# Performance work log

Measured on AMD Instinct MI355X. Metric: run time of the kernel, lower is better.

Reference implementation:

```python
import jax, jax.numpy as jnp
import numpy as np

B, S, D, H = 2, 2048, 1024, 16
HD = D // H  # head_size = 64

def setup_inputs() -> dict:
    key = jax.random.key(0)
    ks = jax.random.split(key, 8)
    sc = 0.02
    return {
        "q": jax.random.normal(ks[0], (B, S, D), jnp.float32),
        "k": jax.random.normal(ks[1], (B, S, D), jnp.float32),
        "v": jax.random.normal(ks[2], (B, S, D), jnp.float32),
        "padding_mask": jnp.zeros((B, 1, 1, S), jnp.float32),
        "Wq": jax.random.normal(ks[3], (D, D), jnp.float32) * sc,
        "bq": jnp.zeros((D,), jnp.float32),
        "Wk": jax.random.normal(ks[4], (D, D), jnp.float32) * sc,
        "bk": jnp.zeros((D,), jnp.float32),
        "Wv": jax.random.normal(ks[5], (D, D), jnp.float32) * sc,
        "bv": jnp.zeros((D,), jnp.float32),
        "Wo": jax.random.normal(ks[6], (D, D), jnp.float32) * sc,
        "bo": jnp.zeros((D,), jnp.float32),
    }

def reference(q, k, v, padding_mask, Wq, bq, Wk, bk, Wv, bv, Wo, bo):
    b = q.shape[0]
    qh = (q @ Wq + bq).reshape(b, -1, H, HD)
    kh = (k @ Wk + bk).reshape(b, -1, H, HD)
    vh = (v @ Wv + bv).reshape(b, -1, H, HD)
    # [B, H, Sq, Sk] scores, materialized as in the original
    qk = jnp.einsum('bjhd,bkhd->bhjk', qh, kh) / jnp.sqrt(jnp.float32(HD))
    qk = qk + padding_mask * -1e12
    attn = jax.nn.softmax(qk, axis=-1)
    qkv = jnp.einsum('bhjk,bkhd->bjhd', attn, vh).reshape(b, -1, D)
    return qkv @ Wo + bo
```

## Files before the change

### kernel.cpp

```cpp
#include <hip/hip_runtime.h>
#include <math.h>

typedef __bf16 bf16_t;
typedef __bf16 bf16x8 __attribute__((ext_vector_type(8)));
typedef __bf16 bf16x4v __attribute__((ext_vector_type(4)));
typedef float f32x4 __attribute__((ext_vector_type(4)));

#define LOG2E 1.4426950408889634f

#if __has_builtin(__builtin_amdgcn_exp2f)
#define EXP2F(x) __builtin_amdgcn_exp2f(x)
#else
#define EXP2F(x) exp2f(x)
#endif

typedef __attribute__((address_space(1))) const unsigned int g_u32;
typedef __attribute__((address_space(3))) unsigned int l_u32;
__device__ __forceinline__ void load_lds_16B(const void* g, void* l){
  __builtin_amdgcn_global_load_lds((g_u32*)g, (l_u32*)l, 16, 0, 0);
}

__global__ __launch_bounds__(256) void wtrans4_kernel(const float* __restrict__ Wq,
                                                      const float* __restrict__ Wk,
                                                      const float* __restrict__ Wv,
                                                      const float* __restrict__ Wo,
                                                      bf16_t* __restrict__ Wcat,
                                                      bf16_t* __restrict__ Wot){
  __shared__ float T[32][33];
  int z = blockIdx.z;
  const float* W = (z == 0) ? Wq : (z == 1) ? Wk : (z == 2) ? Wv : Wo;
  bf16_t* dst = (z < 3) ? (Wcat + (size_t)z * 1024 * 1024) : Wot;
  int x = threadIdx.x, y = threadIdx.y;
  int k0 = blockIdx.y * 32, n0 = blockIdx.x * 32;
  #pragma unroll
  for (int i = 0; i < 4; i++) T[y + 8*i][x] = W[(size_t)(k0 + y + 8*i) * 1024 + n0 + x];
  __syncthreads();
  #pragma unroll
  for (int i = 0; i < 4; i++) dst[(size_t)(n0 + y + 8*i) * 1024 + k0 + x] = (bf16_t)T[x][y + 8*i];
}

__global__ __launch_bounds__(256) void gemm_qkv(const float* __restrict__ qi,
                                                const float* __restrict__ ki,
                                                const float* __restrict__ vi,
                                                const bf16_t* __restrict__ Wcat,
                                                const float* __restrict__ bq,
                                                const float* __restrict__ bk,
                                                const float* __restrict__ bv,
                                                bf16_t* __restrict__ Cqkv){
  const int K = 1024, CS = 3072;
  __shared__ __align__(16) float  Asf[128*32];
  __shared__ __align__(16) bf16_t Bs[128*32];
  int tid = threadIdx.x, wave = tid >> 6, lane = tid & 63;
  int l16 = lane & 15, lq = lane >> 4;
  int n0g = blockIdx.x * 128;
  int seg = n0g >> 10;
  const float* A    = (seg == 0) ? qi : (seg == 1) ? ki : vi;
  const float* bias = (seg == 0) ? bq : (seg == 1) ? bk : bv;
  float scale = (seg == 0) ? 0.125f : 1.0f;
  int m0 = blockIdx.y * 128;
  int wm = (wave >> 1) * 64, wn = (wave & 1) * 64;
  int cposR = lq ^ ((l16 >> 2) & 3);
  int ca0 = (2*lq)     ^ (l16 & 7);
  int ca1 = (2*lq + 1) ^ (l16 & 7);
  f32x4 acc[4][4] = {};
  for (int kt = 0; kt < K; kt += 32){
    __syncthreads();
    #pragma unroll
    for (int i = 0; i < 4; i++){
      int u = tid + 256*i;
      int r = u >> 3, cpos = u & 7, cg = cpos ^ (r & 7);
      load_lds_16B(&A[(size_t)(m0 + r) * K + kt + cg*4], (char*)Asf + (wave*64 + 256*i)*16);
    }
    #pragma unroll
    for (int i = 0; i < 2; i++){
      int u = tid + 256*i;
      int r = u >> 2, cpos = u & 3, cg = cpos ^ ((r >> 2) & 3);
      load_lds_16B(&Wcat[(size_t)(n0g + r) * K + kt + cg*8], (char*)Bs + (wave*64 + 256*i)*16);
    }
    __syncthreads();
    bf16x8 af[4], bfr[4];
    #pragma unroll
    for (int t = 0; t < 4; t++){
      int row = wm + t*16 + l16;
      f32x4 x0 = *reinterpret_cast<f32x4*>(&Asf[row*32 + ca0*4]);
      f32x4 x1 = *reinterpret_cast<f32x4*>(&Asf[row*32 + ca1*4]);
      bf16x8 a;
      a[0] = (bf16_t)x0[0]; a[1] = (bf16_t)x0[1]; a[2] = (bf16_t)x0[2]; a[3] = (bf16_t)x0[3];
      a[4] = (bf16_t)x1[0]; a[5] = (bf16_t)x1[1]; a[6] = (bf16_t)x1[2]; a[7] = (bf16_t)x1[3];
      af[t] = a;
    }
    #pragma unroll
    for (int t = 0; t < 4; t++) bfr[t] = *reinterpret_cast<bf16x8*>(&Bs[(wn + t*16 + l16)*32 + cposR*8]);
    #pragma unroll
    for (int ti = 0; ti < 4; ti++)
      #pragma unroll
      for (int tj = 0; tj < 4; tj++)
        acc[ti][tj] = __builtin_amdgcn_mfma_f32_16x16x32_bf16(af[ti], bfr[tj], acc[ti][tj], 0, 0, 0);
  }
  #pragma unroll
  for (int ti = 0; ti < 4; ti++){
    #pragma unroll
    for (int tj = 0; tj < 4; tj++){
      int col = n0g + wn + tj*16 + l16;
      float bvv = bias[col & 1023];
      #pragma unroll
      for (int r = 0; r < 4; r++){
        int row = m0 + wm + ti*16 + lq*4 + r;
        Cqkv[(size_t)row * CS + col] = (bf16_t)((acc[ti][tj][r] + bvv) * scale);
      }
    }
  }
}

__global__ __launch_bounds__(256) void gemm_out(const bf16_t* __restrict__ A,
                                                const bf16_t* __restrict__ Bt,
                                                const float* __restrict__ bias,
                                                float* __restrict__ C){
  const int K = 1024, N = 1024;
  __shared__ __align__(16) bf16_t As[128*32];
  __shared__ __align__(16) bf16_t Bs[64*32];
  int tid = threadIdx.x, wave = tid >> 6, lane = tid & 63;
  int l16 = lane & 15, lq = lane >> 4;
  int m0 = blockIdx.y * 128, n0 = blockIdx.x * 64;
  int wm = wave * 32;
  int cposR = lq ^ ((l16 >> 2) & 3);
  f32x4 acc[2][4] = {};
  for (int kt = 0; kt < K; kt += 32){
    __syncthreads();
    #pragma unroll
    for (int i = 0; i < 2; i++){
      int u = tid + 256*i;
      int r = u >> 2, cpos = u & 3, cg = cpos ^ ((r >> 2) & 3);
      load_lds_16B(&A[(size_t)(m0 + r) * K + kt + cg*8], (char*)As + (wave*64 + 256*i)*16);
    }
    {
      int r = tid >> 2, cpos = tid & 3, cg = cpos ^ ((r >> 2) & 3);
      load_lds_16B(&Bt[(size_t)(n0 + r) * K + kt + cg*8], (char*)Bs + (wave*64)*16);
    }
    __syncthreads();
    bf16x8 af[2], bfr[4];
    #pragma unroll
    for (int t = 0; t < 2; t++) af[t]  = *reinterpret_cast<bf16x8*>(&As[(wm + t*16 + l16)*32 + cposR*8]);
    #pragma unroll
    for (int t = 0; t < 4; t++) bfr[t] = *reinterpret_cast<bf16x8*>(&Bs[(t*16 + l16)*32 + cposR*8]);
    #pragma unroll
    for (int ti = 0; ti < 2; ti++)
      #pragma unroll
      for (int tj = 0; tj < 4; tj++)
        acc[ti][tj] = __builtin_amdgcn_mfma_f32_16x16x32_bf16(af[ti], bfr[tj], acc[ti][tj], 0, 0, 0);
  }
  #pragma unroll
  for (int ti = 0; ti < 2; ti++){
    #pragma unroll
    for (int tj = 0; tj < 4; tj++){
      int col = n0 + tj*16 + l16;
      float bvv = bias[col];
      #pragma unroll
      for (int r = 0; r < 4; r++){
        int row = m0 + wm + ti*16 + lq*4 + r;
        C[(size_t)row * N + col] = acc[ti][tj][r] + bvv;
      }
    }
  }
}

__global__ __launch_bounds__(256) void vtrans_kernel(const bf16_t* __restrict__ qkv,
                                                     bf16_t* __restrict__ Vt){
  __shared__ bf16_t T[64][72];
  int tid = threadIdx.x;
  int s0 = blockIdx.x * 64, h = blockIdx.y, b = blockIdx.z;
  #pragma unroll
  for (int i = 0; i < 2; i++){
    int u = tid + 256*i;
    int r = u >> 3, c = (u & 7) * 8;
    *reinterpret_cast<uint4*>(&T[r][c]) =
      *reinterpret_cast<const uint4*>(&qkv[(size_t)(b*2048 + s0 + r) * 3072 + 2048 + h*64 + c]);
  }
  __syncthreads();
  #pragma unroll
  for (int i = 0; i < 2; i++){
    int u = tid + 256*i;
    int d = u >> 3, cs = (u & 7) * 8;
    bf16_t t8[8];
    #pragma unroll
    for (int j = 0; j < 8; j++) t8[j] = T[cs + j][d];
    *reinterpret_cast<uint4*>(&Vt[(size_t)((b*16 + h)*64 + d) * 2048 + s0 + cs]) =
      *reinterpret_cast<uint4*>(t8);
  }
}

__global__ __launch_bounds__(256) void attn_kernel(const bf16_t* __restrict__ qkv,
                                                   const bf16_t* __restrict__ vt,
                                                   const float* __restrict__ mask,
                                                   bf16_t* __restrict__ ctx){
  const int S = 2048, DS = 3072, D = 1024, HD = 64;
  __shared__ __align__(16) char smem[67584];
  bf16_t* Qs  = (bf16_t*)smem;
  bf16_t* Ps  = (bf16_t*)smem;
  bf16_t* Ks  = (bf16_t*)(smem + 34816);
  bf16_t* Vts = (bf16_t*)(smem + 51200);
  int tid = threadIdx.x, wave = tid >> 6, lane = tid & 63;
  int l16 = lane & 15, lq = lane >> 4;
  int qt = blockIdx.x, h = blockIdx.y, b = blockIdx.z;
  const bf16_t* Qg = qkv + (size_t)b*S*DS + h*HD;
  const bf16_t* Kg = qkv + (size_t)b*S*DS + 1024 + h*HD;
  const bf16_t* Vg = vt + (size_t)(b*16 + h)*HD*S;

  #pragma unroll
  for (int i = 0; i < 4; i++){
    int u = tid + 256*i;
    int r = u >> 3, cpos = u & 7, cg = cpos ^ (r & 7);
    load_lds_16B(&Qg[(size_t)(qt*128 + r) * DS + cg*8], smem + (wave*64 + 256*i)*16);
  }
  __syncthreads();
  bf16x8 qf[2][2];
  #pragma unroll
  for (int ti = 0; ti < 2; ti++)
    #pragma unroll
    for (int kk = 0; kk < 2; kk++){
      int row = wave*32 + ti*16 + l16;
      int cpos = (kk*4 + lq) ^ (l16 & 7);
      qf[ti][kk] = *reinterpret_cast<bf16x8*>(&Qs[row*64 + cpos*8]);
    }
  f32x4 o[2][4] = {};
  f32x4 ol[2] = {};
  bf16x8 ones;
  #pragma unroll
  for (int j = 0; j < 8; j++) ones[j] = (bf16_t)1.0f;

  for (int kt = 0; kt < S; kt += 128){
    __syncthreads();
    #pragma unroll
    for (int i = 0; i < 4; i++){
      int u = tid + 256*i;
      int r = u >> 3, cpos = u & 7, cg = cpos ^ (r & 7);
      load_lds_16B(&Kg[(size_t)(kt + r) * DS + cg*8], (char*)Ks + (wave*64 + 256*i)*16);
    }
    #pragma unroll
    for (int i = 0; i < 4; i++){
      int u = tid + 256*i;
      int r = u >> 4, cpos = u & 15, cg = cpos ^ (r & 15);
      load_lds_16B(&Vg[(size_t)r * S + kt + cg*8], (char*)Vts + (wave*64 + 256*i)*16);
    }
    __syncthreads();

    f32x4 sc[2][8];
    #pragma unroll
    for (int kk = 0; kk < 2; kk++){
      bf16x8 kf[8];
      #pragma unroll
      for (int tj = 0; tj < 8; tj++){
        int row = tj*16 + l16;
        int cpos = (kk*4 + lq) ^ (l16 & 7);
        kf[tj] = *reinterpret_cast<bf16x8*>(&Ks[row*64 + cpos*8]);
      }
      #pragma unroll
      for (int ti = 0; ti < 2; ti++)
        #pragma unroll
        for (int tj = 0; tj < 8; tj++){
          if (kk == 0){
            f32x4 z = {0.f, 0.f, 0.f, 0.f};
            sc[ti][tj] = __builtin_amdgcn_mfma_f32_16x16x32_bf16(kf[tj], qf[ti][0], z, 0, 0, 0);
          } else {
            sc[ti][tj] = __builtin_amdgcn_mfma_f32_16x16x32_bf16(kf[tj], qf[ti][1], sc[ti][tj], 0, 0, 0);
          }
        }
    }
    float4 mb4[8];
    #pragma unroll
    for (int tj = 0; tj < 8; tj++){
      float4 mv = *reinterpret_cast<const float4*>(&mask[(size_t)b*S + kt + tj*16 + lq*4]);
      mb4[tj].x = mv.x * (-1e12f * LOG2E); mb4[tj].y = mv.y * (-1e12f * LOG2E);
      mb4[tj].z = mv.z * (-1e12f * LOG2E); mb4[tj].w = mv.w * (-1e12f * LOG2E);
    }
    #pragma unroll
    for (int ti = 0; ti < 2; ti++){
      int prow = wave*32 + ti*16 + l16;
      #pragma unroll
      for (int tj = 0; tj < 8; tj++){
        float p0 = EXP2F(fmaf(sc[ti][tj][0], LOG2E, mb4[tj].x));
        float p1 = EXP2F(fmaf(sc[ti][tj][1], LOG2E, mb4[tj].y));
        float p2 = EXP2F(fmaf(sc[ti][tj][2], LOG2E, mb4[tj].z));
        float p3 = EXP2F(fmaf(sc[ti][tj][3], LOG2E, mb4[tj].w));
        bf16x4v w;
        w[0] = (bf16_t)p0; w[1] = (bf16_t)p1; w[2] = (bf16_t)p2; w[3] = (bf16_t)p3;
        *reinterpret_cast<bf16x4v*>(&Ps[prow*136 + tj*16 + lq*4]) = w;
      }
    }
    #pragma unroll
    for (int kk = 0; kk < 4; kk++){
      bf16x8 pf[2], vf[4];
      #pragma unroll
      for (int ti = 0; ti < 2; ti++)
        pf[ti] = *reinterpret_cast<bf16x8*>(&Ps[(wave*32 + ti*16 + l16)*136 + kk*32 + lq*8]);
      #pragma unroll
      for (int dj = 0; dj < 4; dj++){
        int row = dj*16 + l16;
        int cpos = (kk*4 + lq) ^ l16;
        vf[dj] = *reinterpret_cast<bf16x8*>(&Vts[row*128 + cpos*8]);
      }
      #pragma unroll
      for (int ti = 0; ti < 2; ti++){
        #pragma unroll
        for (int dj = 0; dj < 4; dj++)
          o[ti][dj] = __builtin_amdgcn_mfma_f32_16x16x32_bf16(pf[ti], vf[dj], o[ti][dj], 0, 0, 0);
        ol[ti] = __builtin_amdgcn_mfma_f32_16x16x32_bf16(pf[ti], ones, ol[ti], 0, 0, 0);
      }
    }
  }
  #pragma unroll
  for (int ti = 0; ti < 2; ti++){
    #pragma unroll
    for (int r = 0; r < 4; r++){
      float linv = 1.f / ol[ti][r];
      int row = qt*128 + wave*32 + ti*16 + lq*4 + r;
      #pragma unroll
      for (int dj = 0; dj < 4; dj++)
        ctx[(size_t)(b*S + row) * D + h*HD + dj*16 + l16] = (bf16_t)(o[ti][dj][r] * linv);
    }
  }
}

extern "C" void kernel_launch(void* const* d_in, const int* in_sizes, int n_in,
                              void* d_out, int out_size, void* d_ws, size_t ws_size,
                              hipStream_t stream){
  const float* q    = (const float*)d_in[0];
  const float* k    = (const float*)d_in[1];
  const float* v    = (const float*)d_in[2];
  const float* mask = (const float*)d_in[3];
  const float* Wq   = (const float*)d_in[4];
  const float* bq   = (const float*)d_in[5];
  const float* Wk   = (const float*)d_in[6];
  const float* bk   = (const float*)d_in[7];
  const float* Wv   = (const float*)d_in[8];
  const float* bv   = (const float*)d_in[9];
  const float* Wo   = (const float*)d_in[10];
  const float* bo   = (const float*)d_in[11];

  char* ws = (char*)d_ws;
  bf16_t* qkv  = (bf16_t*)(ws);
  bf16_t* Wcat = (bf16_t*)(ws + 25165824);
  bf16_t* Wot  = (bf16_t*)(ws + 31457280);
  bf16_t* Vt   = (bf16_t*)(ws + 33554432);
  bf16_t* ctx  = (bf16_t*)(ws + 41943040);

  wtrans4_kernel<<<dim3(32,32,4), dim3(32,8), 0, stream>>>(Wq, Wk, Wv, Wo, Wcat, Wot);
  gemm_qkv<<<dim3(24,32), 256, 0, stream>>>(q, k, v, Wcat, bq, bk, bv, qkv);
  vtrans_kernel<<<dim3(32,16,2), 256, 0, stream>>>(qkv, Vt);
  attn_kernel<<<dim3(16,16,2), 256, 0, stream>>>(qkv, Vt, mask, ctx);
  gemm_out<<<dim3(16,32), 256, 0, stream>>>(ctx, Wot, bo, (float*)d_out);
}
```

Before: 263.2 us.

## Pre-cast QKV inputs to bf16, shrink attention tiles, deepen out-GEMM K-step

Adds a cast kernel that converts q/k/v to bf16 so the QKV GEMM can load both operands with direct global-to-LDS 16B loads. This path runs only when the workspace is large enough, otherwise the old f32 path is kept. The attention kernel moves to 64-row query tiles and 64-key steps with much smaller LDS, doubling the grid to raise occupancy. The output GEMM uses a 64-wide K step to halve the number of barriers. The cost is an extra pass over the inputs, and the attention kernel gets less reuse of each K/V tile.

```diff
diff --git a/kernel.cpp b/kernel.cpp
--- a/kernel.cpp
+++ b/kernel.cpp
@@ -18,6 +18,19 @@
 typedef __attribute__((address_space(3))) unsigned int l_u32;
 __device__ __forceinline__ void load_lds_16B(const void* g, void* l){
   __builtin_amdgcn_global_load_lds((g_u32*)g, (l_u32*)l, 16, 0, 0);
+}
+
+__global__ __launch_bounds__(256) void cast3_kernel(const float* __restrict__ q,
+                                                    const float* __restrict__ k,
+                                                    const float* __restrict__ v,
+                                                    bf16_t* __restrict__ out){
+  int z = blockIdx.y;
+  const float* x = (z == 0) ? q : (z == 1) ? k : v;
+  int i = blockIdx.x * 256 + threadIdx.x;
+  float4 f = reinterpret_cast<const float4*>(x)[i];
+  bf16x4v w;
+  w[0] = (bf16_t)f.x; w[1] = (bf16_t)f.y; w[2] = (bf16_t)f.z; w[3] = (bf16_t)f.w;
+  reinterpret_cast<bf16x4v*>(out + (size_t)z * 4194304)[i] = w;
 }
 
 __global__ __launch_bounds__(256) void wtrans4_kernel(const float* __restrict__ Wq,
@@ -39,14 +52,71 @@
   for (int i = 0; i < 4; i++) dst[(size_t)(n0 + y + 8*i) * 1024 + k0 + x] = (bf16_t)T[x][y + 8*i];
 }
 
-__global__ __launch_bounds__(256) void gemm_qkv(const float* __restrict__ qi,
-                                                const float* __restrict__ ki,
-                                                const float* __restrict__ vi,
-                                                const bf16_t* __restrict__ Wcat,
-                                                const float* __restrict__ bq,
-                                                const float* __restrict__ bk,
-                                                const float* __restrict__ bv,
-                                                bf16_t* __restrict__ Cqkv){
+__global__ __launch_bounds__(256) void gemm_qkv_bf(const bf16_t* __restrict__ qkvin,
+                                                   const bf16_t* __restrict__ Wcat,
+                                                   const float* __restrict__ bq,
+                                                   const float* __restrict__ bk,
+                                                   const float* __restrict__ bv,
+                                                   bf16_t* __restrict__ Cqkv){
+  const int K = 1024, CS = 3072;
+  __shared__ __align__(16) bf16_t As[128*32];
+  __shared__ __align__(16) bf16_t Bs[128*32];
+  int tid = threadIdx.x, wave = tid >> 6, lane = tid & 63;
+  int l16 = lane & 15, lq = lane >> 4;
+  int n0g = blockIdx.x * 128;
+  int seg = n0g >> 10;
+  const bf16_t* A   = qkvin + (size_t)seg * 4194304;
+  const float* bias = (seg == 0) ? bq : (seg == 1) ? bk : bv;
+  float scale = (seg == 0) ? 0.125f : 1.0f;
+  int m0 = blockIdx.y * 128;
+  int wm = (wave >> 1) * 64, wn = (wave & 1) * 64;
+  int cposR = lq ^ ((l16 >> 2) & 3);
+  f32x4 acc[4][4] = {};
+  for (int kt = 0; kt < K; kt += 32){
+    __syncthreads();
+    #pragma unroll
+    for (int i = 0; i < 2; i++){
+      int u = tid + 256*i;
+      int r = u >> 2, cpos = u & 3, cg = cpos ^ ((r >> 2) & 3);
+      int ldsoff = (wave*64 + 256*i) * 16;
+      load_lds_16B(&A[(size_t)(m0 + r) * K + kt + cg*8], (char*)As + ldsoff);
+      load_lds_16B(&Wcat[(size_t)(n0g + r) * K + kt + cg*8], (char*)Bs + ldsoff);
+    }
+    __syncthreads();
+    bf16x8 af[4], bfr[4];
+    #pragma unroll
+    for (int t = 0; t < 4; t++) af[t]  = *reinterpret_cast<bf16x8*>(&As[(wm + t*16 + l16)*32 + cposR*8]);
+    #pragma unroll
+    for (int t = 0; t < 4; t++) bfr[t] = *reinterpret_cast<bf16x8*>(&Bs[(wn + t*16 + l16)*32 + cposR*8]);
+    #pragma unroll
+    for (int ti = 0; ti < 4; ti++)
+      #pragma unroll
+      for (int tj = 0; tj < 4; tj++)
+        acc[ti][tj] = __builtin_amdgcn_mfma_f32_16x16x32_bf16(af[ti], bfr[tj], acc[ti][tj], 0, 0, 0);
+  }
+  #pragma unroll
+  for (int ti = 0; ti < 4; ti++){
+    #pragma unroll
+    for (int tj = 0; tj < 4; tj++){
+      int col = n0g + wn + tj*16 + l16;
+      float bvv = bias[col & 1023];
+      #pragma unroll
+      for (int r = 0; r < 4; r++){
+        int row = m0 + wm + ti*16 + lq*4 + r;
+        Cqkv[(size_t)row * CS + col] = (bf16_t)((acc[ti][tj][r] + bvv) * scale);
+      }
+    }
+  }
+}
+
+__global__ __launch_bounds__(256) void gemm_qkv_f32(const float* __restrict__ qi,
+                                                    const float* __restrict__ ki,
+                                                    const float* __restrict__ vi,
+                                                    const bf16_t* __restrict__ Wcat,
+                                                    const float* __restrict__ bq,
+                                                    const float* __restrict__ bk,
+                                                    const float* __restrict__ bv,
+                                                    bf16_t* __restrict__ Cqkv){
   const int K = 1024, CS = 3072;
   __shared__ __align__(16) float  Asf[128*32];
   __shared__ __align__(16) bf16_t Bs[128*32];
@@ -117,37 +187,47 @@
                                                 const float* __restrict__ bias,
                                                 float* __restrict__ C){
   const int K = 1024, N = 1024;
-  __shared__ __align__(16) bf16_t As[128*32];
-  __shared__ __align__(16) bf16_t Bs[64*32];
+  __shared__ __align__(16) bf16_t As[128*64];
+  __shared__ __align__(16) bf16_t Bs[64*64];
   int tid = threadIdx.x, wave = tid >> 6, lane = tid & 63;
   int l16 = lane & 15, lq = lane >> 4;
   int m0 = blockIdx.y * 128, n0 = blockIdx.x * 64;
   int wm = wave * 32;
-  int cposR = lq ^ ((l16 >> 2) & 3);
   f32x4 acc[2][4] = {};
-  for (int kt = 0; kt < K; kt += 32){
-    __syncthreads();
+  for (int kt = 0; kt < K; kt += 64){
+    __syncthreads();
+    #pragma unroll
+    for (int i = 0; i < 4; i++){
+      int u = tid + 256*i;
+      int r = u >> 3, cpos = u & 7, cg = cpos ^ (r & 7);
+      load_lds_16B(&A[(size_t)(m0 + r) * K + kt + cg*8], (char*)As + (wave*64 + 256*i)*16);
+    }
     #pragma unroll
     for (int i = 0; i < 2; i++){
       int u = tid + 256*i;
-      int r = u >> 2, cpos = u & 3, cg = cpos ^ ((r >> 2) & 3);
-      load_lds_16B(&A[(size_t)(m0 + r) * K + kt + cg*8], (char*)As + (wave*64 + 256*i)*16);
-    }
-    {
-      int r = tid >> 2, cpos = tid & 3, cg = cpos ^ ((r >> 2) & 3);
-      load_lds_16B(&Bt[(size_t)(n0 + r) * K + kt + cg*8], (char*)Bs + (wave*64)*16);
-    }
-    __syncthreads();
-    bf16x8 af[2], bfr[4];
-    #pragma unroll
-    for (int t = 0; t < 2; t++) af[t]  = *reinterpret_cast<bf16x8*>(&As[(wm + t*16 + l16)*32 + cposR*8]);
-    #pragma unroll
-    for (int t = 0; t < 4; t++) bfr[t] = *reinterpret_cast<bf16x8*>(&Bs[(t*16 + l16)*32 + cposR*8]);
-    #pragma unroll
-    for (int ti = 0; ti < 2; ti++)
-      #pragma unroll
-      for (int tj = 0; tj < 4; tj++)
-        acc[ti][tj] = __builtin_amdgcn_mfma_f32_16x16x32_bf16(af[ti], bfr[tj], acc[ti][tj], 0, 0, 0);
+      int r = u >> 3, cpos = u & 7, cg = cpos ^ (r & 7);
+      load_lds_16B(&Bt[(size_t)(n0 + r) * K + kt + cg*8], (char*)Bs + (wave*64 + 256*i)*16);
+    }
+    __syncthreads();
+    #pragma unroll
+    for (int kk = 0; kk < 2; kk++){
+      bf16x8 af[2], bfr[4];
+      #pragma unroll
+      for (int t = 0; t < 2; t++){
+        int row = wm + t*16 + l16, cpos = (kk*4 + lq) ^ (l16 & 7);
+        af[t] = *reinterpret_cast<bf16x8*>(&As[row*64 + cpos*8]);
+      }
+      #pragma unroll
+      for (int t = 0; t < 4; t++){
+        int row = t*16 + l16, cpos = (kk*4 + lq) ^ (l16 & 7);
+        bfr[t] = *reinterpret_cast<bf16x8*>(&Bs[row*64 + cpos*8]);
+      }
+      #pragma unroll
+      for (int ti = 0; ti < 2; ti++)
+        #pragma unroll
+        for (int tj = 0; tj < 4; tj++)
+          acc[ti][tj] = __builtin_amdgcn_mfma_f32_16x16x32_bf16(af[ti], bfr[tj], acc[ti][tj], 0, 0, 0);
+    }
   }
   #pragma unroll
   for (int ti = 0; ti < 2; ti++){
@@ -194,11 +274,11 @@
                                                    const float* __restrict__ mask,
                                                    bf16_t* __restrict__ ctx){
   const int S = 2048, DS = 3072, D = 1024, HD = 64;
-  __shared__ __align__(16) char smem[67584];
+  __shared__ __align__(16) char smem[25600];
   bf16_t* Qs  = (bf16_t*)smem;
   bf16_t* Ps  = (bf16_t*)smem;
-  bf16_t* Ks  = (bf16_t*)(smem + 34816);
-  bf16_t* Vts = (bf16_t*)(smem + 51200);
+  bf16_t* Ks  = (bf16_t*)(smem + 9216);
+  bf16_t* Vts = (bf16_t*)(smem + 17408);
   int tid = threadIdx.x, wave = tid >> 6, lane = tid & 63;
   int l16 = lane & 15, lq = lane >> 4;
   int qt = blockIdx.x, h = blockIdx.y, b = blockIdx.z;
@@ -207,117 +287,96 @@
   const bf16_t* Vg = vt + (size_t)(b*16 + h)*HD*S;
 
   #pragma unroll
-  for (int i = 0; i < 4; i++){
+  for (int i = 0; i < 2; i++){
     int u = tid + 256*i;
     int r = u >> 3, cpos = u & 7, cg = cpos ^ (r & 7);
-    load_lds_16B(&Qg[(size_t)(qt*128 + r) * DS + cg*8], smem + (wave*64 + 256*i)*16);
+    load_lds_16B(&Qg[(size_t)(qt*64 + r) * DS + cg*8], smem + (wave*64 + 256*i)*16);
   }
   __syncthreads();
-  bf16x8 qf[2][2];
-  #pragma unroll
-  for (int ti = 0; ti < 2; ti++)
-    #pragma unroll
-    for (int kk = 0; kk < 2; kk++){
-      int row = wave*32 + ti*16 + l16;
-      int cpos = (kk*4 + lq) ^ (l16 & 7);
-      qf[ti][kk] = *reinterpret_cast<bf16x8*>(&Qs[row*64 + cpos*8]);
-    }
-  f32x4 o[2][4] = {};
-  f32x4 ol[2] = {};
+  bf16x8 qf[2];
+  #pragma unroll
+  for (int kk = 0; kk < 2; kk++){
+    int row = wave*16 + l16;
+    int cpos = (kk*4 + lq) ^ (l16 & 7);
+    qf[kk] = *reinterpret_cast<bf16x8*>(&Qs[row*64 + cpos*8]);
+  }
+  f32x4 o[4] = {};
+  f32x4 ol = {};
   bf16x8 ones;
   #pragma unroll
   for (int j = 0; j < 8; j++) ones[j] = (bf16_t)1.0f;
 
-  for (int kt = 0; kt < S; kt += 128){
-    __syncthreads();
-    #pragma unroll
-    for (int i = 0; i < 4; i++){
+  for (int kt = 0; kt < S; kt += 64){
+    __syncthreads();
+    #pragma unroll
+    for (int i = 0; i < 2; i++){
       int u = tid + 256*i;
       int r = u >> 3, cpos = u & 7, cg = cpos ^ (r & 7);
       load_lds_16B(&Kg[(size_t)(kt + r) * DS + cg*8], (char*)Ks + (wave*64 + 256*i)*16);
     }
     #pragma unroll
-    for (int i = 0; i < 4; i++){
-      int u = tid + 256*i;
-      int r = u >> 4, cpos = u & 15, cg = cpos ^ (r & 15);
+    for (int i = 0; i < 2; i++){
+      int u = tid + 256*i;
+      int r = u >> 3, cpos = u & 7, cg = cpos ^ (r & 7);
       load_lds_16B(&Vg[(size_t)r * S + kt + cg*8], (char*)Vts + (wave*64 + 256*i)*16);
     }
     __syncthreads();
 
-    f32x4 sc[2][8];
+    f32x4 sc[4];
     #pragma unroll
     for (int kk = 0; kk < 2; kk++){
-      bf16x8 kf[8];
-      #pragma unroll
-      for (int tj = 0; tj < 8; tj++){
+      bf16x8 kf[4];
+      #pragma unroll
+      for (int tj = 0; tj < 4; tj++){
         int row = tj*16 + l16;
         int cpos = (kk*4 + lq) ^ (l16 & 7);
         kf[tj] = *reinterpret_cast<bf16x8*>(&Ks[row*64 + cpos*8]);
       }
       #pragma unroll
-      for (int ti = 0; ti < 2; ti++)
-        #pragma unroll
-        for (int tj = 0; tj < 8; tj++){
-          if (kk == 0){
-            f32x4 z = {0.f, 0.f, 0.f, 0.f};
-            sc[ti][tj] = __builtin_amdgcn_mfma_f32_16x16x32_bf16(kf[tj], qf[ti][0], z, 0, 0, 0);
-          } else {
-            sc[ti][tj] = __builtin_amdgcn_mfma_f32_16x16x32_bf16(kf[tj], qf[ti][1], sc[ti][tj], 0, 0, 0);
-          }
+      for (int tj = 0; tj < 4; tj++){
+        if (kk == 0){
+          f32x4 z = {0.f, 0.f, 0.f, 0.f};
+          sc[tj] = __builtin_amdgcn_mfma_f32_16x16x32_bf16(kf[tj], qf[0], z, 0, 0, 0);
+        } else {
+          sc[tj] = __builtin_amdgcn_mfma_f32_16x16x32_bf16(kf[tj], qf[1], sc[tj], 0, 0, 0);
         }
-    }
-    float4 mb4[8];
-    #pragma unroll
-    for (int tj = 0; tj < 8; tj++){
+      }
+    }
+    int prow = wave*16 + l16;
+    #pragma unroll
+    for (int tj = 0; tj < 4; tj++){
       float4 mv = *reinterpret_cast<const float4*>(&mask[(size_t)b*S + kt + tj*16 + lq*4]);
-      mb4[tj].x = mv.x * (-1e12f * LOG2E); mb4[tj].y = mv.y * (-1e12f * LOG2E);
-      mb4[tj].z = mv.z * (-1e12f * LOG2E); mb4[tj].w = mv.w * (-1e12f * LOG2E);
-    }
-    #pragma unroll
-    for (int ti = 0; ti < 2; ti++){
-      int prow = wave*32 + ti*16 + l16;
-      #pragma unroll
-      for (int tj = 0; tj < 8; tj++){
-        float p0 = EXP2F(fmaf(sc[ti][tj][0], LOG2E, mb4[tj].x));
-        float p1 = EXP2F(fmaf(sc[ti][tj][1], LOG2E, mb4[tj].y));
-        float p2 = EXP2F(fmaf(sc[ti][tj][2], LOG2E, mb4[tj].z));
-        float p3 = EXP2F(fmaf(sc[ti][tj][3], LOG2E, mb4[tj].w));
-        bf16x4v w;
-        w[0] = (bf16_t)p0; w[1] = (bf16_t)p1; w[2] = (bf16_t)p2; w[3] = (bf16_t)p3;
-        *reinterpret_cast<bf16x4v*>(&Ps[prow*136 + tj*16 + lq*4]) = w;
-      }
-    }
-    #pragma unroll
-    for (int kk = 0; kk < 4; kk++){
-      bf16x8 pf[2], vf[4];
-      #pragma unroll
-      for (int ti = 0; ti < 2; ti++)
-        pf[ti] = *reinterpret_cast<bf16x8*>(&Ps[(wave*32 + ti*16 + l16)*136 + kk*32 + lq*8]);
+      float p0 = EXP2F(fmaf(sc[tj][0], LOG2E, mv.x * (-1e12f * LOG2E)));
+      float p1 = EXP2F(fmaf(sc[tj][1], LOG2E, mv.y * (-1e12f * LOG2E)));
+      float p2 = EXP2F(fmaf(sc[tj][2], LOG2E, mv.z * (-1e12f * LOG2E)));
+      float p3 = EXP2F(fmaf(sc[tj][3], LOG2E, mv.w * (-1e12f * LOG2E)));
+      bf16x4v w;
+      w[0] = (bf16_t)p0; w[1] = (bf16_t)p1; w[2] = (bf16_t)p2; w[3] = (bf16_t)p3;
+      *reinterpret_cast<bf16x4v*>(&Ps[prow*72 + tj*16 + lq*4]) = w;
+    }
+    #pragma unroll
+    for (int kk = 0; kk < 2; kk++){
+      bf16x8 pf = *reinterpret_cast<bf16x8*>(&Ps[(wave*16 + l16)*72 + kk*32 + lq*8]);
+      bf16x8 vf[4];
       #pragma unroll
       for (int dj = 0; dj < 4; dj++){
         int row = dj*16 + l16;
-        int cpos = (kk*4 + lq) ^ l16;
-        vf[dj] = *reinterpret_cast<bf16x8*>(&Vts[row*128 + cpos*8]);
-      }
-      #pragma unroll
-      for (int ti = 0; ti < 2; ti++){
-        #pragma unroll
-        for (int dj = 0; dj < 4; dj++)
-          o[ti][dj] = __builtin_amdgcn_mfma_f32_16x16x32_bf16(pf[ti], vf[dj], o[ti][dj], 0, 0, 0);
-        ol[ti] = __builtin_amdgcn_mfma_f32_16x16x32_bf16(pf[ti], ones, ol[ti], 0, 0, 0);
-      }
-    }
-  }
-  #pragma unroll
-  for (int ti = 0; ti < 2; ti++){
-    #pragma unroll
-    for (int r = 0; r < 4; r++){
-      float linv = 1.f / ol[ti][r];
-      int row = qt*128 + wave*32 + ti*16 + lq*4 + r;
+        int cpos = (kk*4 + lq) ^ (l16 & 7);
+        vf[dj] = *reinterpret_cast<bf16x8*>(&Vts[row*64 + cpos*8]);
+      }
       #pragma unroll
       for (int dj = 0; dj < 4; dj++)
-        ctx[(size_t)(b*S + row) * D + h*HD + dj*16 + l16] = (bf16_t)(o[ti][dj][r] * linv);
-    }
+        o[dj] = __builtin_amdgcn_mfma_f32_16x16x32_bf16(pf, vf[dj], o[dj], 0, 0, 0);
+      ol = __builtin_amdgcn_mfma_f32_16x16x32_bf16(pf, ones, ol, 0, 0, 0);
+    }
+  }
+  #pragma unroll
+  for (int r = 0; r < 4; r++){
+    float linv = 1.f / ol[r];
+    int row = qt*64 + wave*16 + lq*4 + r;
+    #pragma unroll
+    for (int dj = 0; dj < 4; dj++)
+      ctx[(size_t)(b*S + row) * D + h*HD + dj*16 + l16] = (bf16_t)(o[dj][r] * linv);
   }
 }
 
@@ -338,15 +397,21 @@
   const float* bo   = (const float*)d_in[11];
 
   char* ws = (char*)d_ws;
-  bf16_t* qkv  = (bf16_t*)(ws);
-  bf16_t* Wcat = (bf16_t*)(ws + 25165824);
-  bf16_t* Wot  = (bf16_t*)(ws + 31457280);
-  bf16_t* Vt   = (bf16_t*)(ws + 33554432);
-  bf16_t* ctx  = (bf16_t*)(ws + 41943040);
+  bf16_t* qkv   = (bf16_t*)(ws);
+  bf16_t* Wcat  = (bf16_t*)(ws + 25165824);
+  bf16_t* Wot   = (bf16_t*)(ws + 31457280);
+  bf16_t* Vt    = (bf16_t*)(ws + 33554432);
+  bf16_t* ctx   = (bf16_t*)(ws + 41943040);
+  bf16_t* qkvin = (bf16_t*)(ws + 33554432);
 
   wtrans4_kernel<<<dim3(32,32,4), dim3(32,8), 0, stream>>>(Wq, Wk, Wv, Wo, Wcat, Wot);
-  gemm_qkv<<<dim3(24,32), 256, 0, stream>>>(q, k, v, Wcat, bq, bk, bv, qkv);
+  if (ws_size >= 58720256){
+    cast3_kernel<<<dim3(4096,3), 256, 0, stream>>>(q, k, v, qkvin);
+    gemm_qkv_bf<<<dim3(24,32), 256, 0, stream>>>(qkvin, Wcat, bq, bk, bv, qkv);
+  } else {
+    gemm_qkv_f32<<<dim3(24,32), 256, 0, stream>>>(q, k, v, Wcat, bq, bk, bv, qkv);
+  }
   vtrans_kernel<<<dim3(32,16,2), 256, 0, stream>>>(qkv, Vt);
-  attn_kernel<<<dim3(16,16,2), 256, 0, stream>>>(qkv, Vt, mask, ctx);
+  attn_kernel<<<dim3(32,16,2), 256, 0, stream>>>(qkv, Vt, mask, ctx);
   gemm_out<<<dim3(16,32), 256, 0, stream>>>(ctx, Wot, bo, (float*)d_out);
 }
```

Measured after the change: 241.9 us. 1.09x faster.
